# Kernel tuning notes

Hardware: AMD Instinct MI355X
Metric: run time of the kernel (lower is better)

## Reference

```python
import jax, jax.numpy as jnp
import numpy as np

H = 16  # num_heads


def _rotate_half(t):
    d = t.shape[-1] // 2
    return jnp.concatenate((-t[..., d:], t[..., :d]), axis=-1)


def setup_inputs() -> dict:
    key = jax.random.key(0)
    ks = jax.random.split(key, 4)
    S, HID = 2048, 1280
    D = HID // H  # 80
    x = jax.random.normal(ks[0], (S, HID), dtype=jnp.float32)
    # rotary tables (seq_len, head_dim)
    inv_freq = 1.0 / (10000.0 ** (jnp.arange(0, D, 2, dtype=jnp.float32) / D))
    freqs = jnp.arange(S, dtype=jnp.float32)[:, None] * inv_freq[None, :]  # (S, D/2)
    emb = jnp.concatenate([freqs, freqs], axis=-1)  # (S, D)
    cos = jnp.cos(emb)
    sin = jnp.sin(emb)
    W_qkv = jax.random.normal(ks[1], (HID, 3 * HID), dtype=jnp.float32) * 0.02
    b_qkv = jnp.zeros((3 * HID,), dtype=jnp.float32)
    W_out = jax.random.normal(ks[2], (HID, HID), dtype=jnp.float32) * 0.02
    b_out = jnp.zeros((HID,), dtype=jnp.float32)
    # 8 windows of 256 tokens each -> block-diagonal attention
    cu_seqlens = jnp.arange(0, S + 1, 256, dtype=jnp.int32)  # (9,)
    return {"x": x, "cos": cos, "sin": sin, "W_qkv": W_qkv, "b_qkv": b_qkv,
            "W_out": W_out, "b_out": b_out, "cu_seqlens": cu_seqlens}


def _segment_mask(cu_seqlens, seq_len, dtype):
    positions = jnp.arange(seq_len)
    starts = cu_seqlens[:-1]
    ends = cu_seqlens[1:]
    in_segment = (positions[:, None] >= starts[None, :]) & (positions[:, None] < ends[None, :])
    segment_ids = jnp.argmax(in_segment.astype(jnp.int32), axis=-1)  # (S,)
    same_segment = segment_ids[:, None] == segment_ids[None, :]      # (S, S)
    return jnp.where(same_segment, jnp.zeros((), dtype), jnp.finfo(dtype).min)


def reference(x, cos, sin, W_qkv, b_qkv, W_out, b_out, cu_seqlens):
    S, HID = x.shape
    D = HID // H
    scale = D ** -0.5
    qkv = x @ W_qkv + b_qkv                       # (S, 3*HID)
    q, k, v = jnp.split(qkv, 3, axis=-1)
    q = q.reshape(S, H, D)
    k = k.reshape(S, H, D)
    v = v.reshape(S, H, D)
    cos_f = cos[:, :D][:, None, :]                # (S, 1, D)
    sin_f = sin[:, :D][:, None, :]
    q = q * cos_f + _rotate_half(q) * sin_f       # inline RoPE (fp32)
    k = k * cos_f + _rotate_half(k) * sin_f
    q = jnp.transpose(q, (1, 0, 2))               # (H, S, D)
    k = jnp.transpose(k, (1, 0, 2))
    v = jnp.transpose(v, (1, 0, 2))
    scores = jnp.einsum('hqd,hkd->hqk', q, k) * scale  # (H, S, S)
    mask = _segment_mask(cu_seqlens, S, scores.dtype)  # (S, S) block-diagonal bias
    scores = scores + mask[None, :, :]
    weights = jax.nn.softmax(scores, axis=-1)
    out = jnp.einsum('hqk,hkd->hqd', weights, v)       # (H, S, D)
    out = jnp.transpose(out, (1, 0, 2)).reshape(S, HID)
    return out @ W_out + b_out
```

## Files before the change

### kernel.cpp

```cpp
#include <hip/hip_runtime.h>


typedef short s16x8 __attribute__((ext_vector_type(8)));
typedef __bf16 bf16x8 __attribute__((ext_vector_type(8)));
typedef float f32x4 __attribute__((ext_vector_type(4)));
typedef unsigned short u16;
typedef unsigned long long u64;

__device__ __forceinline__ f32x4 mfma16(s16x8 a, s16x8 b, f32x4 c) {
  return __builtin_amdgcn_mfma_f32_16x16x32_bf16(
      __builtin_bit_cast(bf16x8, a), __builtin_bit_cast(bf16x8, b), c, 0, 0, 0);
}
__device__ __forceinline__ u16 f2b(float f) {
  union { float f; unsigned u; } v;
  v.f = f;
  unsigned r = v.u + 0x7fffu + ((v.u >> 16) & 1u);
  return (u16)(r >> 16);
}
__device__ __forceinline__ void gl16(const u16* g, u16* l) {
  __builtin_amdgcn_global_load_lds(
      (const __attribute__((address_space(1))) unsigned int*)(const void*)g,
      (__attribute__((address_space(3))) unsigned int*)(void*)l, 16, 0, 0);
}

__device__ __forceinline__ void transpose_body(const float* __restrict__ W,
                                               u16* __restrict__ WT, int K, int N,
                                               int nb, int kb, int t, float (*tile)[33]) {
  int tx = t & 31, ty = t >> 5;
#pragma unroll
  for (int r = 0; r < 32; r += 8)
    tile[ty + r][tx] = W[(long)(kb + ty + r) * N + nb + tx];
  __syncthreads();
#pragma unroll
  for (int r = 0; r < 32; r += 8)
    WT[(long)(nb + ty + r) * K + kb + tx] = f2b(tile[tx][ty + r]);
}

__global__ __launch_bounds__(256) void prep(const float* __restrict__ x,
                                            u16* __restrict__ xb,
                                            const float* __restrict__ Wqkv,
                                            u16* __restrict__ WqkvT,
                                            const float* __restrict__ Wout,
                                            u16* __restrict__ WoutT) {
  __shared__ float tile[32][33];
  int bid = blockIdx.x, t = threadIdx.x;
  if (bid < 2560) {
    int i = bid * 256 + t;
    float4 v = ((const float4*)x)[i];
    u64 pk = (u64)f2b(v.x) | ((u64)f2b(v.y) << 16) | ((u64)f2b(v.z) << 32) |
             ((u64)f2b(v.w) << 48);
    ((u64*)xb)[i] = pk;
  } else if (bid < 7360) {
    int i = bid - 2560;
    transpose_body(Wqkv, WqkvT, 1280, 3840, (i % 120) * 32, (i / 120) * 32, t, tile);
  } else {
    int i = bid - 7360;
    transpose_body(Wout, WoutT, 1280, 1280, (i % 40) * 32, (i / 40) * 32, t, tile);
  }
}

__global__ __launch_bounds__(256) void gemm_qkv_rope(const u16* __restrict__ A,
                                                     const u16* __restrict__ B,
                                                     const float* __restrict__ bias,
                                                     const float* __restrict__ cosb,
                                                     const float* __restrict__ sinb,
                                                     u16* __restrict__ Qr,
                                                     u16* __restrict__ Kr,
                                                     u16* __restrict__ VT) {
  __shared__ u16 As[64 * 32];
  __shared__ u16 Bs[160 * 32];
  const int K = 1280;
  int n0 = blockIdx.x * 160, m0 = blockIdx.y * 64;
  int t = threadIdx.x, w = t >> 6, lane = t & 63, lm = lane & 15, quad = lane >> 4;
  int koff = quad * 8;
  int wm = (w >> 1) * 32, wn = (w & 1) * 80;
  int srow = t >> 2, scol = (t & 3) * 8;
  const u16* Ag = A + (long)(m0 + srow) * K + scol;
  const u16* Bg = B + (long)(n0 + srow) * K + scol;
  const u16* Bg3 = B + (long)(n0 + 128 + srow) * K + scol;
  u16* AsW = As + w * 512;
  u16* BsW = Bs + w * 512;
  u16* BsW2 = Bs + 2048 + w * 512;
  u16* BsW3 = Bs + 4096 + w * 512;
  f32x4 acc[2][5] = {};
  for (int k0 = 0; k0 < K; k0 += 32) {
    __syncthreads();
    gl16(Ag + k0, AsW);
    gl16(Bg + k0, BsW);
    gl16(Bg + (long)64 * K + k0, BsW2);
    if (t < 128) gl16(Bg3 + k0, BsW3);
    __syncthreads();
    s16x8 af[2], bfr[5];
#pragma unroll
    for (int mt = 0; mt < 2; mt++)
      af[mt] = *(const s16x8*)&As[(wm + mt * 16 + lm) * 32 + koff];
#pragma unroll
    for (int nt = 0; nt < 5; nt++)
      bfr[nt] = *(const s16x8*)&Bs[(wn + nt * 16 + lm) * 32 + koff];
#pragma unroll
    for (int mt = 0; mt < 2; mt++)
#pragma unroll
      for (int nt = 0; nt < 5; nt++)
        acc[mt][nt] = mfma16(af[mt], bfr[nt], acc[mt][nt]);
  }

  int region = n0 / 1280;
  int hcol = (n0 - region * 1280 + wn) / 80;
  float bv[5];
#pragma unroll
  for (int nt = 0; nt < 5; nt++) bv[nt] = bias[n0 + wn + nt * 16 + lm];

  if (region == 2) {
#pragma unroll
    for (int mt = 0; mt < 2; mt++) {
      int sbase = m0 + wm + mt * 16 + quad * 4;
#pragma unroll
      for (int nt = 0; nt < 5; nt++) {
        int d = nt * 16 + lm;
        u64 pk = 0;
#pragma unroll
        for (int r = 0; r < 4; r++)
          pk |= (u64)f2b(acc[mt][nt][r] + bv[nt]) << (16 * r);
        *(u64*)&VT[((long)hcol * 80 + d) * 2048 + sbase] = pk;
      }
    }
    return;
  }

  const float scale = 0.111803398874989f;
  bool lo = lm < 8;
  u16* Out = (region == 0) ? Qr : Kr;
  float oscale = (region == 0) ? scale : 1.0f;
#pragma unroll
  for (int mt = 0; mt < 2; mt++)
#pragma unroll
    for (int r = 0; r < 4; r++) {
      int s = m0 + wm + mt * 16 + quad * 4 + r;
      float val[5], sw[5];
#pragma unroll
      for (int nt = 0; nt < 5; nt++) val[nt] = acc[mt][nt][r] + bv[nt];
#pragma unroll
      for (int nt = 0; nt < 5; nt++) sw[nt] = __shfl_xor(val[nt], 8);
      float rot[5];
      rot[0] = -(lo ? sw[2] : sw[3]);
      rot[1] = -(lo ? sw[3] : sw[4]);
      rot[2] = lo ? -sw[4] : sw[0];
      rot[3] = lo ? sw[0] : sw[1];
      rot[4] = lo ? sw[1] : sw[2];
      u16* orow = Out + ((long)hcol * 2048 + s) * 80;
      const float* crow = cosb + s * 80;
      const float* srw = sinb + s * 80;
#pragma unroll
      for (int nt = 0; nt < 5; nt++) {
        int d = nt * 16 + lm;
        orow[d] = f2b((val[nt] * crow[d] + rot[nt] * srw[d]) * oscale);
      }
    }
}

template <bool OUT_F32>
__global__ __launch_bounds__(256) void gemm_bt(const u16* __restrict__ A,
                                               const u16* __restrict__ B,
                                               const float* __restrict__ bias,
                                               void* __restrict__ Cout,
                                               int M, int N, int K) {
  __shared__ u16 As[64 * 32];
  __shared__ u16 Bs[128 * 32];
  int m0 = blockIdx.y * 64, n0 = blockIdx.x * 128;
  int t = threadIdx.x;
  int w = t >> 6, lane = t & 63, lm = lane & 15, quad = lane >> 4;
  int koff = quad * 8;
  int wm = (w >> 1) * 32, wn = (w & 1) * 64;
  int srow = t >> 2, scol = (t & 3) * 8;
  const u16* Ag = A + (long)(m0 + srow) * K + scol;
  const u16* Bg = B + (long)(n0 + srow) * K + scol;
  u16* AsW = As + w * 512;
  u16* BsW = Bs + w * 512;
  u16* BsW2 = Bs + 2048 + w * 512;
  f32x4 acc[2][4] = {};
  for (int k0 = 0; k0 < K; k0 += 32) {
    __syncthreads();
    gl16(Ag + k0, AsW);
    gl16(Bg + k0, BsW);
    gl16(Bg + (long)64 * K + k0, BsW2);
    __syncthreads();
    s16x8 af[2], bf[4];
#pragma unroll
    for (int mt = 0; mt < 2; mt++)
      af[mt] = *(const s16x8*)&As[(wm + mt * 16 + lm) * 32 + koff];
#pragma unroll
    for (int nt = 0; nt < 4; nt++)
      bf[nt] = *(const s16x8*)&Bs[(wn + nt * 16 + lm) * 32 + koff];
#pragma unroll
    for (int mt = 0; mt < 2; mt++)
#pragma unroll
      for (int nt = 0; nt < 4; nt++)
        acc[mt][nt] = mfma16(af[mt], bf[nt], acc[mt][nt]);
  }
#pragma unroll
  for (int mt = 0; mt < 2; mt++)
#pragma unroll
    for (int nt = 0; nt < 4; nt++) {
      int col = n0 + wn + nt * 16 + lm;
      float bvv = bias[col];
#pragma unroll
      for (int r = 0; r < 4; r++) {
        int row = m0 + wm + mt * 16 + quad * 4 + r;
        float v = acc[mt][nt][r] + bvv;
        if (OUT_F32) ((float*)Cout)[(long)row * N + col] = v;
        else ((u16*)Cout)[(long)row * N + col] = f2b(v);
      }
    }
}

__global__ __launch_bounds__(256, 1) void attn_kernel(const u16* __restrict__ Qr,
                                                      const u16* __restrict__ Kr,
                                                      const u16* __restrict__ VT,
                                                      u16* __restrict__ AO) {
  int qh = blockIdx.x, seg = blockIdx.y, h = blockIdx.z;
  int t = threadIdx.x;
  int w = t >> 6, lane = t & 63, lm = lane & 15, quad = lane >> 4;
  __shared__ u16 Ps[4][32 * 256];

  int s0 = seg * 256 + qh * 128 + w * 32;
  const u16* Qh = Qr + ((long)h * 2048 + s0) * 80;
  const u16* Kh = Kr + ((long)h * 2048 + seg * 256) * 80;

  f32x4 sc[2][16] = {};
  s16x8 zz = {};
#pragma unroll
  for (int kk = 0; kk < 3; kk++) {
    int dbase = kk * 32 + quad * 8;
    bool valid = dbase < 80;
    s16x8 af[2];
#pragma unroll
    for (int mt = 0; mt < 2; mt++)
      af[mt] = valid ? *(const s16x8*)(Qh + (mt * 16 + lm) * 80 + dbase) : zz;
#pragma unroll
    for (int nt = 0; nt < 16; nt++) {
      s16x8 bfr = valid ? *(const s16x8*)(Kh + (nt * 16 + lm) * 80 + dbase) : zz;
#pragma unroll
      for (int mt = 0; mt < 2; mt++)
        sc[mt][nt] = mfma16(af[mt], bfr, sc[mt][nt]);
    }
  }

  float rowinv[8];
#pragma unroll
  for (int mt = 0; mt < 2; mt++)
#pragma unroll
    for (int r = 0; r < 4; r++) {
      float m = sc[mt][0][r];
#pragma unroll
      for (int nt = 1; nt < 16; nt++) m = fmaxf(m, sc[mt][nt][r]);
      m = fmaxf(m, __shfl_xor(m, 1));
      m = fmaxf(m, __shfl_xor(m, 2));
      m = fmaxf(m, __shfl_xor(m, 4));
      m = fmaxf(m, __shfl_xor(m, 8));
      float s = 0.f;
#pragma unroll
      for (int nt = 0; nt < 16; nt++) {
        float e = __expf(sc[mt][nt][r] - m);
        sc[mt][nt][r] = e;
        s += e;
      }
      s += __shfl_xor(s, 1);
      s += __shfl_xor(s, 2);
      s += __shfl_xor(s, 4);
      s += __shfl_xor(s, 8);
      rowinv[mt * 4 + r] = 1.0f / s;
      int row = mt * 16 + quad * 4 + r;
#pragma unroll
      for (int nt = 0; nt < 16; nt++) {
        int chunk = nt * 2 + (lm >> 3);
        Ps[w][row * 256 + ((chunk ^ row) << 3) + (lm & 7)] = f2b(sc[mt][nt][r]);
      }
    }
  asm volatile("s_waitcnt lgkmcnt(0)" ::: "memory");

  f32x4 oacc[2][5] = {};
  const u16* Vh = VT + (long)h * 80 * 2048 + seg * 256;
#pragma unroll
  for (int kc = 0; kc < 8; kc++) {
    s16x8 pa[2];
#pragma unroll
    for (int mt = 0; mt < 2; mt++) {
      int row = mt * 16 + lm;
      pa[mt] = *(const s16x8*)&Ps[w][row * 256 + (((kc * 4 + quad) ^ row) << 3)];
    }
#pragma unroll
    for (int nt = 0; nt < 5; nt++) {
      s16x8 bvv = *(const s16x8*)(Vh + (long)(nt * 16 + lm) * 2048 + kc * 32 + quad * 8);
#pragma unroll
      for (int mt = 0; mt < 2; mt++)
        oacc[mt][nt] = mfma16(pa[mt], bvv, oacc[mt][nt]);
    }
  }
#pragma unroll
  for (int mt = 0; mt < 2; mt++)
#pragma unroll
    for (int nt = 0; nt < 5; nt++)
#pragma unroll
      for (int r = 0; r < 4; r++)
        AO[(long)(s0 + mt * 16 + quad * 4 + r) * 1280 + h * 80 + nt * 16 + lm] =
            f2b(oacc[mt][nt][r] * rowinv[mt * 4 + r]);
}

extern "C" void kernel_launch(void* const* d_in, const int* in_sizes, int n_in,
                              void* d_out, int out_size, void* d_ws, size_t ws_size,
                              hipStream_t stream) {
  const float* x    = (const float*)d_in[0];
  const float* cosb = (const float*)d_in[1];
  const float* sinb = (const float*)d_in[2];
  const float* Wqkv = (const float*)d_in[3];
  const float* bqkv = (const float*)d_in[4];
  const float* Wout = (const float*)d_in[5];
  const float* bout = (const float*)d_in[6];

  char* p = (char*)d_ws;
  u16* xb    = (u16*)p;
  u16* WqkvT = (u16*)(p + 5242880);
  u16* WoutT = (u16*)(p + 15073280);
  u16* Qr    = (u16*)(p + 18350080);
  u16* Kr    = (u16*)(p + 23592960);
  u16* VT    = (u16*)(p + 28835840);
  u16* AO    = xb;

  prep<<<dim3(8960), dim3(256), 0, stream>>>(x, xb, Wqkv, WqkvT, Wout, WoutT);
  gemm_qkv_rope<<<dim3(24, 32), dim3(256), 0, stream>>>(xb, WqkvT, bqkv, cosb, sinb,
                                                        Qr, Kr, VT);
  attn_kernel<<<dim3(2, 8, 16), dim3(256), 0, stream>>>(Qr, Kr, VT, AO);
  gemm_bt<true><<<dim3(10, 32), dim3(256), 0, stream>>>(AO, WoutT, bout, d_out,
                                                        2048, 1280, 1280);
}
```

Before: 173.5 us.

## Drop LDS staging in GEMMs, load MFMA fragments directly, XCD-aware tile mapping

Both GEMMs stop staging tiles through shared memory with barriers. Each wave now loads its MFMA fragments straight from global memory (L2/L1), with the K loop unrolled by 4. Blocks are remapped to 128x80 tiles using an XCD-aware index so blocks on the same XCD share B columns in their L2. This removes the barriers and LDS traffic, at the cost of redundant global loads: the B fragments are fetched separately by every wave, and the reads are narrow and strided.

```diff
diff --git a/kernel.cpp b/kernel.cpp
--- a/kernel.cpp
+++ b/kernel.cpp
@@ -16,11 +16,6 @@
   v.f = f;
   unsigned r = v.u + 0x7fffu + ((v.u >> 16) & 1u);
   return (u16)(r >> 16);
-}
-__device__ __forceinline__ void gl16(const u16* g, u16* l) {
-  __builtin_amdgcn_global_load_lds(
-      (const __attribute__((address_space(1))) unsigned int*)(const void*)g,
-      (__attribute__((address_space(3))) unsigned int*)(void*)l, 16, 0, 0);
 }
 
 __device__ __forceinline__ void transpose_body(const float* __restrict__ W,
@@ -67,53 +62,42 @@
                                                      u16* __restrict__ Qr,
                                                      u16* __restrict__ Kr,
                                                      u16* __restrict__ VT) {
-  __shared__ u16 As[64 * 32];
-  __shared__ u16 Bs[160 * 32];
   const int K = 1280;
-  int n0 = blockIdx.x * 160, m0 = blockIdx.y * 64;
+  int i = blockIdx.x;
+  int xcd = i & 7, j = i >> 3;
+  int n0 = (xcd * 6 + (j % 6)) * 80;
+  int m0 = (j / 6) * 128;
   int t = threadIdx.x, w = t >> 6, lane = t & 63, lm = lane & 15, quad = lane >> 4;
-  int koff = quad * 8;
-  int wm = (w >> 1) * 32, wn = (w & 1) * 80;
-  int srow = t >> 2, scol = (t & 3) * 8;
-  const u16* Ag = A + (long)(m0 + srow) * K + scol;
-  const u16* Bg = B + (long)(n0 + srow) * K + scol;
-  const u16* Bg3 = B + (long)(n0 + 128 + srow) * K + scol;
-  u16* AsW = As + w * 512;
-  u16* BsW = Bs + w * 512;
-  u16* BsW2 = Bs + 2048 + w * 512;
-  u16* BsW3 = Bs + 4096 + w * 512;
+  int mw = m0 + w * 32;
+  const u16* Ab = A + (long)(mw + lm) * K + quad * 8;
+  const u16* Bb = B + (long)(n0 + lm) * K + quad * 8;
   f32x4 acc[2][5] = {};
+#pragma unroll 4
   for (int k0 = 0; k0 < K; k0 += 32) {
-    __syncthreads();
-    gl16(Ag + k0, AsW);
-    gl16(Bg + k0, BsW);
-    gl16(Bg + (long)64 * K + k0, BsW2);
-    if (t < 128) gl16(Bg3 + k0, BsW3);
-    __syncthreads();
-    s16x8 af[2], bfr[5];
-#pragma unroll
-    for (int mt = 0; mt < 2; mt++)
-      af[mt] = *(const s16x8*)&As[(wm + mt * 16 + lm) * 32 + koff];
+    s16x8 af[2], bf[5];
+#pragma unroll
+    for (int mt = 0; mt < 2; mt++)
+      af[mt] = *(const s16x8*)(Ab + (long)mt * 16 * K + k0);
 #pragma unroll
     for (int nt = 0; nt < 5; nt++)
-      bfr[nt] = *(const s16x8*)&Bs[(wn + nt * 16 + lm) * 32 + koff];
+      bf[nt] = *(const s16x8*)(Bb + (long)nt * 16 * K + k0);
 #pragma unroll
     for (int mt = 0; mt < 2; mt++)
 #pragma unroll
       for (int nt = 0; nt < 5; nt++)
-        acc[mt][nt] = mfma16(af[mt], bfr[nt], acc[mt][nt]);
+        acc[mt][nt] = mfma16(af[mt], bf[nt], acc[mt][nt]);
   }
 
   int region = n0 / 1280;
-  int hcol = (n0 - region * 1280 + wn) / 80;
+  int hcol = (n0 - region * 1280) / 80;
   float bv[5];
 #pragma unroll
-  for (int nt = 0; nt < 5; nt++) bv[nt] = bias[n0 + wn + nt * 16 + lm];
+  for (int nt = 0; nt < 5; nt++) bv[nt] = bias[n0 + nt * 16 + lm];
 
   if (region == 2) {
 #pragma unroll
     for (int mt = 0; mt < 2; mt++) {
-      int sbase = m0 + wm + mt * 16 + quad * 4;
+      int sbase = mw + mt * 16 + quad * 4;
 #pragma unroll
       for (int nt = 0; nt < 5; nt++) {
         int d = nt * 16 + lm;
@@ -135,7 +119,7 @@
   for (int mt = 0; mt < 2; mt++)
 #pragma unroll
     for (int r = 0; r < 4; r++) {
-      int s = m0 + wm + mt * 16 + quad * 4 + r;
+      int s = mw + mt * 16 + quad * 4 + r;
       float val[5], sw[5];
 #pragma unroll
       for (int nt = 0; nt < 5; nt++) val[nt] = acc[mt][nt][r] + bv[nt];
@@ -158,57 +142,45 @@
     }
 }
 
-template <bool OUT_F32>
-__global__ __launch_bounds__(256) void gemm_bt(const u16* __restrict__ A,
-                                               const u16* __restrict__ B,
-                                               const float* __restrict__ bias,
-                                               void* __restrict__ Cout,
-                                               int M, int N, int K) {
-  __shared__ u16 As[64 * 32];
-  __shared__ u16 Bs[128 * 32];
-  int m0 = blockIdx.y * 64, n0 = blockIdx.x * 128;
-  int t = threadIdx.x;
-  int w = t >> 6, lane = t & 63, lm = lane & 15, quad = lane >> 4;
-  int koff = quad * 8;
-  int wm = (w >> 1) * 32, wn = (w & 1) * 64;
-  int srow = t >> 2, scol = (t & 3) * 8;
-  const u16* Ag = A + (long)(m0 + srow) * K + scol;
-  const u16* Bg = B + (long)(n0 + srow) * K + scol;
-  u16* AsW = As + w * 512;
-  u16* BsW = Bs + w * 512;
-  u16* BsW2 = Bs + 2048 + w * 512;
-  f32x4 acc[2][4] = {};
+__global__ __launch_bounds__(256) void gemm_out(const u16* __restrict__ A,
+                                                const u16* __restrict__ B,
+                                                const float* __restrict__ bias,
+                                                float* __restrict__ C) {
+  const int K = 1280, N = 1280;
+  int i = blockIdx.x;
+  int xcd = i & 7, j = i >> 3;
+  int n0 = (xcd * 2 + (j & 1)) * 80;
+  int m0 = (j >> 1) * 128;
+  int t = threadIdx.x, w = t >> 6, lane = t & 63, lm = lane & 15, quad = lane >> 4;
+  int mw = m0 + w * 32;
+  const u16* Ab = A + (long)(mw + lm) * K + quad * 8;
+  const u16* Bb = B + (long)(n0 + lm) * K + quad * 8;
+  f32x4 acc[2][5] = {};
+#pragma unroll 4
   for (int k0 = 0; k0 < K; k0 += 32) {
-    __syncthreads();
-    gl16(Ag + k0, AsW);
-    gl16(Bg + k0, BsW);
-    gl16(Bg + (long)64 * K + k0, BsW2);
-    __syncthreads();
-    s16x8 af[2], bf[4];
-#pragma unroll
-    for (int mt = 0; mt < 2; mt++)
-      af[mt] = *(const s16x8*)&As[(wm + mt * 16 + lm) * 32 + koff];
-#pragma unroll
-    for (int nt = 0; nt < 4; nt++)
-      bf[nt] = *(const s16x8*)&Bs[(wn + nt * 16 + lm) * 32 + koff];
-#pragma unroll
-    for (int mt = 0; mt < 2; mt++)
-#pragma unroll
-      for (int nt = 0; nt < 4; nt++)
+    s16x8 af[2], bf[5];
+#pragma unroll
+    for (int mt = 0; mt < 2; mt++)
+      af[mt] = *(const s16x8*)(Ab + (long)mt * 16 * K + k0);
+#pragma unroll
+    for (int nt = 0; nt < 5; nt++)
+      bf[nt] = *(const s16x8*)(Bb + (long)nt * 16 * K + k0);
+#pragma unroll
+    for (int mt = 0; mt < 2; mt++)
+#pragma unroll
+      for (int nt = 0; nt < 5; nt++)
         acc[mt][nt] = mfma16(af[mt], bf[nt], acc[mt][nt]);
   }
 #pragma unroll
   for (int mt = 0; mt < 2; mt++)
 #pragma unroll
-    for (int nt = 0; nt < 4; nt++) {
-      int col = n0 + wn + nt * 16 + lm;
+    for (int nt = 0; nt < 5; nt++) {
+      int col = n0 + nt * 16 + lm;
       float bvv = bias[col];
 #pragma unroll
       for (int r = 0; r < 4; r++) {
-        int row = m0 + wm + mt * 16 + quad * 4 + r;
-        float v = acc[mt][nt][r] + bvv;
-        if (OUT_F32) ((float*)Cout)[(long)row * N + col] = v;
-        else ((u16*)Cout)[(long)row * N + col] = f2b(v);
+        int row = mw + mt * 16 + quad * 4 + r;
+        C[(long)row * N + col] = acc[mt][nt][r] + bvv;
       }
     }
 }
@@ -327,9 +299,8 @@
   u16* AO    = xb;
 
   prep<<<dim3(8960), dim3(256), 0, stream>>>(x, xb, Wqkv, WqkvT, Wout, WoutT);
-  gemm_qkv_rope<<<dim3(24, 32), dim3(256), 0, stream>>>(xb, WqkvT, bqkv, cosb, sinb,
-                                                        Qr, Kr, VT);
+  gemm_qkv_rope<<<dim3(768), dim3(256), 0, stream>>>(xb, WqkvT, bqkv, cosb, sinb,
+                                                     Qr, Kr, VT);
   attn_kernel<<<dim3(2, 8, 16), dim3(256), 0, stream>>>(Qr, Kr, VT, AO);
-  gemm_bt<true><<<dim3(10, 32), dim3(256), 0, stream>>>(AO, WoutT, bout, d_out,
-                                                        2048, 1280, 1280);
-}
+  gemm_out<<<dim3(256), dim3(256), 0, stream>>>(AO, WoutT, bout, (float*)d_out);
+}
```

After: 254.2 us. +46.6%, slower.
